# Kernel optimization log

Hardware: AMD Instinct MI355X
Metric: run time of the kernel (lower is better)

The kernel has to match this reference:

```python
import jax, jax.numpy as jnp
import numpy as np

B, Z, K, T = 4, 64, 400, 48000
CIN, COUT, KS, DIL = 128, 128, 3, 1
H = 32


def setup_inputs() -> dict:
    key = jax.random.key(0)
    ks = jax.random.split(key, 10)
    s = lambda n: 1.0 / np.sqrt(n)
    return {
        "x": jax.random.normal(ks[0], (B, CIN, T), jnp.float32),
        "z": jax.random.normal(ks[1], (B, Z, K), jnp.float32),
        # weight_model: Conv1d(Z->H, k=1), ReLU, Conv1d(H -> CIN*COUT*KS, k=1)
        "w1": jax.random.normal(ks[2], (H, Z), jnp.float32) * s(Z),
        "b1": jax.random.normal(ks[3], (H,), jnp.float32) * 0.01,
        "w2": jax.random.normal(ks[4], (CIN * COUT * KS, H), jnp.float32) * s(H),
        "b2": jax.random.normal(ks[5], (CIN * COUT * KS,), jnp.float32) * s(CIN * KS),
        # bias_model: Conv1d(Z->H, k=1), ReLU, Conv1d(H -> COUT, k=1)
        "bw1": jax.random.normal(ks[6], (H, Z), jnp.float32) * s(Z),
        "bb1": jax.random.normal(ks[7], (H,), jnp.float32) * 0.01,
        "bw2": jax.random.normal(ks[8], (COUT, H), jnp.float32) * s(H),
        "bb2": jax.random.normal(ks[9], (COUT,), jnp.float32) * 0.01,
    }


def _mlp1x1(z, wa, ba, wb, bb):
    # two pointwise Conv1d layers with ReLU in between; z: [B, Z, K]
    h = jax.nn.relu(jnp.einsum('hz,bzk->bhk', wa, z) + ba[None, :, None])
    return jnp.einsum('oh,bhk->bok', wb, h) + bb[None, :, None]


def _unfold_causal(x, ksize, dil):
    # causal im2col: tap i is x delayed by i*dil samples (left-padded with zeros)
    pad = dil * (ksize - 1)
    xp = jnp.pad(x, ((0, 0), (0, 0), (pad, 0)))
    taps = [xp[:, :, pad - i * dil: pad - i * dil + x.shape[-1]] for i in range(ksize)]
    return jnp.concatenate(taps, axis=1)  # [B, CIN*KS, T]


def reference(x, z, w1, b1, w2, b2, bw1, bb1, bw2, bb2):
    Tk = T // K  # samples per weight chunk
    xu = _unfold_causal(x, KS, DIL)                       # [B, CIN*KS, T]
    xr = xu.transpose(0, 2, 1).reshape(B * K, Tk, CIN * KS)
    w = _mlp1x1(z, w1, b1, w2, b2)                        # [B, CIN*COUT*KS, K]
    w = w.reshape(B, CIN * KS, COUT, K).transpose(0, 3, 1, 2).reshape(B * K, CIN * KS, COUT)
    bias = _mlp1x1(z, bw1, bb1, bw2, bb2)                 # [B, COUT, K]
    bias = bias.transpose(0, 2, 1).reshape(B * K, COUT)
    y = jnp.einsum('btc,bco->bto', xr, w) + bias[:, None, :]
    return y.reshape(B, T, COUT).transpose(0, 2, 1)       # [B, COUT, T]
```

## Files before the change

kernel.cpp:

```cpp
#include <hip/hip_runtime.h>
#include <stdint.h>

#define TT     48000
#define TK     120
#define NC     128
#define NA     384
#define NZ     64
#define NH     32
#define NK     400
#define NCHUNK 1600
#define MW     49152

typedef float f32x4 __attribute__((ext_vector_type(4)));
typedef __bf16 bf16x8 __attribute__((ext_vector_type(8)));

static __device__ __forceinline__ uint16_t f2bf(float f) {
    uint32_t x; __builtin_memcpy(&x, &f, 4);
    return (uint16_t)((x + 0x7fffu + ((x >> 16) & 1u)) >> 16);
}
static __device__ __forceinline__ uint32_t pk2u(uint16_t lo, uint16_t hi) {
    return (uint32_t)lo | ((uint32_t)hi << 16);
}

__global__ __launch_bounds__(256) void k1_hidden(
    const float* __restrict__ z,
    const float* __restrict__ w1, const float* __restrict__ b1,
    const float* __restrict__ bw1, const float* __restrict__ bb1,
    const float* __restrict__ bw2, const float* __restrict__ bb2,
    uint16_t* __restrict__ Hb, float* __restrict__ biasws) {
    int tid = threadIdx.x, lane = tid & 63, w = tid >> 6;
    int chunk0 = blockIdx.x * 4;
    int b = chunk0 / NK;
    int k0 = chunk0 - b * NK;

    __shared__ float w1sT[64][33];
    __shared__ float bw1sT[64][33];
    __shared__ float bw2s[128][33];
    __shared__ float zs[64][4];
    __shared__ float hbs[4][33];
    __shared__ float b1s[32], bb1s[32], bb2s[128];

    {
        int row = tid >> 3, c0 = (tid & 7) * 8;
        float4 a0 = *(const float4*)(w1 + row * NZ + c0);
        float4 a1 = *(const float4*)(w1 + row * NZ + c0 + 4);
        float4 c0v = *(const float4*)(bw1 + row * NZ + c0);
        float4 c1v = *(const float4*)(bw1 + row * NZ + c0 + 4);
        const float av[8] = {a0.x,a0.y,a0.z,a0.w,a1.x,a1.y,a1.z,a1.w};
        const float cv[8] = {c0v.x,c0v.y,c0v.z,c0v.w,c1v.x,c1v.y,c1v.z,c1v.w};
#pragma unroll
        for (int j = 0; j < 8; ++j) {
            w1sT[c0 + j][row]  = av[j];
            bw1sT[c0 + j][row] = cv[j];
        }
    }
    {
        int r = tid >> 1, cb = (tid & 1) * 16;
        float4 v0 = *(const float4*)(bw2 + r * NH + cb);
        float4 v1 = *(const float4*)(bw2 + r * NH + cb + 4);
        float4 v2 = *(const float4*)(bw2 + r * NH + cb + 8);
        float4 v3 = *(const float4*)(bw2 + r * NH + cb + 12);
        const float vv[16] = {v0.x,v0.y,v0.z,v0.w,v1.x,v1.y,v1.z,v1.w,
                              v2.x,v2.y,v2.z,v2.w,v3.x,v3.y,v3.z,v3.w};
#pragma unroll
        for (int j = 0; j < 16; ++j) bw2s[r][cb + j] = vv[j];
    }
    if (tid < 64) {
        float4 zv = *(const float4*)(z + ((size_t)b * NZ + tid) * NK + k0);
        zs[tid][0] = zv.x; zs[tid][1] = zv.y; zs[tid][2] = zv.z; zs[tid][3] = zv.w;
    }
    if (tid < 32) { b1s[tid] = b1[tid]; bb1s[tid] = bb1[tid]; }
    if (tid >= 128 && tid < 256) bb2s[tid - 128] = bb2[tid - 128];
    __syncthreads();

    int chunk = chunk0 + w;
    if (lane < NH) {
        float s = b1s[lane];
#pragma unroll
        for (int i = 0; i < NZ; ++i) s = fmaf(w1sT[i][lane], zs[i][w], s);
        Hb[(size_t)chunk * NH + lane] = f2bf(fmaxf(s, 0.f));
    } else {
        int j = lane - NH;
        float s = bb1s[j];
#pragma unroll
        for (int i = 0; i < NZ; ++i) s = fmaf(bw1sT[i][j], zs[i][w], s);
        hbs[w][j] = fmaxf(s, 0.f);
    }

#pragma unroll
    for (int r = 0; r < 2; ++r) {
        int c = r * 64 + lane;
        float s = bb2s[c];
#pragma unroll
        for (int j = 0; j < NH; ++j) s = fmaf(bw2s[c][j], hbs[w][j], s);
        biasws[(size_t)chunk * NC + c] = s;
    }
}

__global__ __launch_bounds__(256) void k2_wgen(
    const float* __restrict__ w2, const float* __restrict__ b2,
    const uint16_t* __restrict__ Hb, uint16_t* __restrict__ Wt,
    int chunk0, int nchunk) {
    int tid = threadIdx.x, lane = tid & 63, w = tid >> 6;
    int quad = lane >> 4, li = lane & 15;
    __shared__ __align__(16) uint16_t St[4][16][68];
    int mb = blockIdx.x * 256 + w * 64;

    bf16x8 afrag[4];
    float4 bias[4];
#pragma unroll
    for (int t = 0; t < 4; ++t) {
        int mp = mb + t * 16 + li;
        int a = mp % NA, c = mp / NA;
        const float* src = w2 + ((size_t)a * NC + c) * NH + quad * 8;
        float4 v0 = *(const float4*)(src);
        float4 v1 = *(const float4*)(src + 4);
        uint16_t tmp[8] = { f2bf(v0.x), f2bf(v0.y), f2bf(v0.z), f2bf(v0.w),
                            f2bf(v1.x), f2bf(v1.y), f2bf(v1.z), f2bf(v1.w) };
        __builtin_memcpy(&afrag[t], tmp, 16);
        float bv[4];
#pragma unroll
        for (int r = 0; r < 4; ++r) {
            int mpr = mb + t * 16 + quad * 4 + r;
            bv[r] = b2[(size_t)(mpr % NA) * NC + (mpr / NA)];
        }
        bias[t] = make_float4(bv[0], bv[1], bv[2], bv[3]);
    }

    for (int g = 0; g < 10; ++g) {
        int cl0 = blockIdx.y * 160 + g * 16;
        if (cl0 >= nchunk) break;
        int cl = cl0 + li;
        if (cl >= nchunk) cl = nchunk - 1;
        bf16x8 hfrag = *(const bf16x8*)(Hb + (size_t)(chunk0 + cl) * NH + quad * 8);
#pragma unroll
        for (int t = 0; t < 4; ++t) {
            f32x4 acc = {0.f, 0.f, 0.f, 0.f};
            acc = __builtin_amdgcn_mfma_f32_16x16x32_bf16(afrag[t], hfrag, acc, 0, 0, 0);
            uint16_t p[4] = { f2bf(acc[0] + bias[t].x), f2bf(acc[1] + bias[t].y),
                              f2bf(acc[2] + bias[t].z), f2bf(acc[3] + bias[t].w) };
            uint64_t pv; __builtin_memcpy(&pv, p, 8);
            *(uint64_t*)&St[w][li][t * 16 + quad * 4] = pv;
        }
#pragma unroll
        for (int p = 0; p < 2; ++p) {
            int ch = (lane >> 3) + p * 8, part = lane & 7;
            uint4 v = *(const uint4*)&St[w][ch][part * 8];
            int cg = cl0 + ch;
            if (cg < nchunk)
                *(uint4*)(Wt + (size_t)cg * MW + mb + part * 8) = v;
        }
    }
}

__global__ __launch_bounds__(512, 4) void k3_conv(
    const float* __restrict__ x, const uint16_t* __restrict__ Wt,
    const float* __restrict__ biasws, float* __restrict__ out, int chunk0) {
    int cl = blockIdx.x, chunk = chunk0 + cl;
    int b = chunk / NK, k = chunk - b * NK;
    int kbase = k * TK;
    int tid = threadIdx.x, lane = tid & 63, w = tid >> 6;
    int quad = lane >> 4, li = lane & 15;
    int tblk = (w >> 1) * 32, cblk = (w & 1) * 64;

    __shared__ __align__(16) char smem[81920];
    char* Xa  = smem;
    char* Db0 = smem + 32768;
    char* Db1 = smem + 49152;
    char* Db2 = smem + 65536;
    const uint16_t* WtC = Wt + (size_t)cl * MW;

    auto stageD = [&](char* dst, int dks) {
#pragma unroll
        for (int j = 0; j < 2; ++j) {
            int g = (w * 2 + j) * 64 + lane;
            int c = g >> 3, sd = g & 7;
            int o = sd ^ (c & 7);
            const uint16_t* gsrc = WtC + (size_t)c * NA + dks * 64 + o * 8;
            __builtin_amdgcn_global_load_lds(
                (__attribute__((address_space(1))) void*)gsrc,
                (__attribute__((address_space(3))) void*)(dst + (w * 2 + j) * 1024),
                16, 0, 0);
        }
    };

    stageD(Db0, 0);
    stageD(Db1, 1);

    const float* xb = x + (size_t)b * NC * TT;
    {
        int thalf = lane >> 5;
        int tq4 = (lane & 31) * 4;
#pragma unroll
        for (int i = 0; i < 4; ++i) {
            int p = i * 16 + w * 2 + thalf;
            int cin = p * 2;
            int tg = kbase + tq4;
            int tga = tg > TT - 4 ? TT - 4 : tg;
            float4 v0 = *(const float4*)(xb + (size_t)cin * TT + tga);
            float4 v1 = *(const float4*)(xb + (size_t)(cin + 1) * TT + tga);
            uint32_t pks[4] = { pk2u(f2bf(v0.x), f2bf(v1.x)),
                                pk2u(f2bf(v0.y), f2bf(v1.y)),
                                pk2u(f2bf(v0.z), f2bf(v1.z)),
                                pk2u(f2bf(v0.w), f2bf(v1.w)) };
            int q = cin >> 3, wi = (cin & 7) * 2;
#pragma unroll
            for (int j = 0; j < 4; ++j) {
                int r = tq4 + 2 + j;
                if (r < 128)
                    *(uint32_t*)(Xa + r * 256 + ((q ^ (r & 15)) << 4) + wi) = pks[j];
            }
            if (tq4 == 0) {
                uint32_t r0 = 0, r1 = 0;
                if (kbase > 0) {
                    float2 u0 = *(const float2*)(xb + (size_t)cin * TT + kbase - 2);
                    float2 u1 = *(const float2*)(xb + (size_t)(cin + 1) * TT + kbase - 2);
                    r0 = pk2u(f2bf(u0.x), f2bf(u1.x));
                    r1 = pk2u(f2bf(u0.y), f2bf(u1.y));
                }
                *(uint32_t*)(Xa + (q << 4) + wi) = r0;
                *(uint32_t*)(Xa + 256 + ((q ^ 1) << 4) + wi) = r1;
            }
        }
    }
    asm volatile("s_waitcnt lgkmcnt(0)" ::: "memory");

    f32x4 acc[2][4];
#pragma unroll
    for (int i = 0; i < 2; ++i)
#pragma unroll
        for (int j = 0; j < 4; ++j) acc[i][j] = (f32x4){0.f, 0.f, 0.f, 0.f};

#pragma unroll
    for (int dk = 0; dk < 6; ++dk) {
        if (dk < 5) asm volatile("s_waitcnt vmcnt(2)" ::: "memory");
        else        asm volatile("s_waitcnt vmcnt(0)" ::: "memory");
        __builtin_amdgcn_s_barrier();
        __builtin_amdgcn_sched_barrier(0);
        if (dk < 4) {
            int sel = (dk + 2) % 3;
            stageD(sel == 0 ? Db0 : (sel == 1 ? Db1 : Db2), dk + 2);
        }
        int cs = dk % 3;
        char* cur = cs == 0 ? Db0 : (cs == 1 ? Db1 : Db2);
        int tap = dk >> 1;

        bf16x8 bfr[2][4];
#pragma unroll
        for (int s = 0; s < 2; ++s)
#pragma unroll
            for (int ct = 0; ct < 4; ++ct) {
                int c = cblk + ct * 16 + li;
                bfr[s][ct] = *(const bf16x8*)(cur + c * 128
                             + (((s * 4 + quad) ^ (c & 7)) << 4));
            }
#pragma unroll
        for (int s = 0; s < 2; ++s) {
            bf16x8 af[2];
#pragma unroll
            for (int tt = 0; tt < 2; ++tt) {
                int r = tblk + tt * 16 + li + 2 - tap;
                r = r > 127 ? 127 : r;
                int q = (dk & 1) * 8 + s * 4 + quad;
                af[tt] = *(const bf16x8*)(Xa + r * 256 + ((q ^ (r & 15)) << 4));
            }
#pragma unroll
            for (int tt = 0; tt < 2; ++tt)
#pragma unroll
                for (int ct = 0; ct < 4; ++ct)
                    acc[tt][ct] = __builtin_amdgcn_mfma_f32_16x16x32_bf16(
                        af[tt], bfr[s][ct], acc[tt][ct], 0, 0, 0);
        }
    }

#pragma unroll
    for (int ct = 0; ct < 4; ++ct) {
        int c = cblk + ct * 16 + li;
        float bias = biasws[(size_t)chunk * NC + c];
        float* ob = out + ((size_t)b * NC + c) * TT + kbase;
#pragma unroll
        for (int tt = 0; tt < 2; ++tt) {
            int t0v = tblk + tt * 16 + quad * 4;
            if (t0v < TK) {
                f32x4 v = acc[tt][ct];
                *(float4*)(ob + t0v) = make_float4(v[0] + bias, v[1] + bias,
                                                   v[2] + bias, v[3] + bias);
            }
        }
    }
}

extern "C" void kernel_launch(void* const* d_in, const int* in_sizes, int n_in,
                              void* d_out, int out_size, void* d_ws, size_t ws_size,
                              hipStream_t stream) {
    const float* x   = (const float*)d_in[0];
    const float* z   = (const float*)d_in[1];
    const float* w1  = (const float*)d_in[2];
    const float* b1  = (const float*)d_in[3];
    const float* w2  = (const float*)d_in[4];
    const float* b2  = (const float*)d_in[5];
    const float* bw1 = (const float*)d_in[6];
    const float* bb1 = (const float*)d_in[7];
    const float* bw2 = (const float*)d_in[8];
    const float* bb2 = (const float*)d_in[9];
    float* out = (float*)d_out;

    char* ws = (char*)d_ws;
    uint16_t* Hb     = (uint16_t*)(ws);
    float*    biasws = (float*)(ws + 102400);
    const size_t wt_off = 921600;
    uint16_t* Wt     = (uint16_t*)(ws + wt_off);

    size_t avail = (ws_size > wt_off) ? (ws_size - wt_off) : 0;
    int batch = (int)(avail / ((size_t)MW * 2));
    if (batch > 800) batch = 800;
    if (batch < 1) batch = 1;

    k1_hidden<<<NCHUNK / 4, 256, 0, stream>>>(z, w1, b1, bw1, bb1, bw2, bb2, Hb, biasws);

    for (int c0 = 0; c0 < NCHUNK; c0 += batch) {
        int nc = NCHUNK - c0;
        if (nc > batch) nc = batch;
        dim3 g2(MW / 256, (nc + 159) / 160, 1);
        k2_wgen<<<g2, 256, 0, stream>>>(w2, b2, Hb, Wt, c0, nc);
        k3_conv<<<nc, 512, 0, stream>>>(x, Wt, biasws, out, c0);
    }
}
```

Measured before the change: 284.6 us.

## Load conv weights directly into registers, drop LDS weight staging

The conv kernel now reads its per-chunk weight fragments straight from global memory into registers, double-buffered in software across the six K-steps, instead of staging them through three LDS buffers with async global-to-LDS loads and per-step barriers. LDS use falls from 80 KB to 32 KB (only the input tile), and the launch bound is raised to allow 8 blocks per CU. This is meant to remove per-step barriers and LDS traffic and to raise occupancy. In exchange, each wave issues its own global loads for weights (64 channels are duplicated across the four t-block waves), and register pressure goes up.

```diff
diff --git a/kernel.cpp b/kernel.cpp
--- a/kernel.cpp
+++ b/kernel.cpp
@@ -153,7 +153,7 @@
     }
 }
 
-__global__ __launch_bounds__(512, 4) void k3_conv(
+__global__ __launch_bounds__(512, 8) void k3_conv(
     const float* __restrict__ x, const uint16_t* __restrict__ Wt,
     const float* __restrict__ biasws, float* __restrict__ out, int chunk0) {
     int cl = blockIdx.x, chunk = chunk0 + cl;
@@ -163,29 +163,21 @@
     int quad = lane >> 4, li = lane & 15;
     int tblk = (w >> 1) * 32, cblk = (w & 1) * 64;
 
-    __shared__ __align__(16) char smem[81920];
-    char* Xa  = smem;
-    char* Db0 = smem + 32768;
-    char* Db1 = smem + 49152;
-    char* Db2 = smem + 65536;
+    __shared__ __align__(16) char Xa[32768];
     const uint16_t* WtC = Wt + (size_t)cl * MW;
 
-    auto stageD = [&](char* dst, int dks) {
-#pragma unroll
-        for (int j = 0; j < 2; ++j) {
-            int g = (w * 2 + j) * 64 + lane;
-            int c = g >> 3, sd = g & 7;
-            int o = sd ^ (c & 7);
-            const uint16_t* gsrc = WtC + (size_t)c * NA + dks * 64 + o * 8;
-            __builtin_amdgcn_global_load_lds(
-                (__attribute__((address_space(1))) void*)gsrc,
-                (__attribute__((address_space(3))) void*)(dst + (w * 2 + j) * 1024),
-                16, 0, 0);
-        }
-    };
-
-    stageD(Db0, 0);
-    stageD(Db1, 1);
+    const uint16_t* wsrc = WtC + (size_t)(cblk + li) * NA + quad * 8;
+
+#define LOADW(dst, dk)                                                        \
+    _Pragma("unroll")                                                         \
+    for (int s = 0; s < 2; ++s)                                               \
+        _Pragma("unroll")                                                     \
+        for (int ct = 0; ct < 4; ++ct)                                        \
+            dst[s][ct] = *(const bf16x8*)(wsrc + (size_t)ct * 16 * NA         \
+                                          + (dk) * 64 + s * 32);
+
+    bf16x8 w0[2][4], w1[2][4];
+    LOADW(w0, 0);
 
     const float* xb = x + (size_t)b * NC * TT;
     {
@@ -223,7 +215,7 @@
             }
         }
     }
-    asm volatile("s_waitcnt lgkmcnt(0)" ::: "memory");
+    __syncthreads();
 
     f32x4 acc[2][4];
 #pragma unroll
@@ -231,47 +223,33 @@
 #pragma unroll
         for (int j = 0; j < 4; ++j) acc[i][j] = (f32x4){0.f, 0.f, 0.f, 0.f};
 
-#pragma unroll
-    for (int dk = 0; dk < 6; ++dk) {
-        if (dk < 5) asm volatile("s_waitcnt vmcnt(2)" ::: "memory");
-        else        asm volatile("s_waitcnt vmcnt(0)" ::: "memory");
-        __builtin_amdgcn_s_barrier();
-        __builtin_amdgcn_sched_barrier(0);
-        if (dk < 4) {
-            int sel = (dk + 2) % 3;
-            stageD(sel == 0 ? Db0 : (sel == 1 ? Db1 : Db2), dk + 2);
-        }
-        int cs = dk % 3;
-        char* cur = cs == 0 ? Db0 : (cs == 1 ? Db1 : Db2);
-        int tap = dk >> 1;
-
-        bf16x8 bfr[2][4];
-#pragma unroll
-        for (int s = 0; s < 2; ++s)
-#pragma unroll
-            for (int ct = 0; ct < 4; ++ct) {
-                int c = cblk + ct * 16 + li;
-                bfr[s][ct] = *(const bf16x8*)(cur + c * 128
-                             + (((s * 4 + quad) ^ (c & 7)) << 4));
-            }
-#pragma unroll
-        for (int s = 0; s < 2; ++s) {
-            bf16x8 af[2];
-#pragma unroll
-            for (int tt = 0; tt < 2; ++tt) {
-                int r = tblk + tt * 16 + li + 2 - tap;
-                r = r > 127 ? 127 : r;
-                int q = (dk & 1) * 8 + s * 4 + quad;
-                af[tt] = *(const bf16x8*)(Xa + r * 256 + ((q ^ (r & 15)) << 4));
-            }
-#pragma unroll
-            for (int tt = 0; tt < 2; ++tt)
-#pragma unroll
-                for (int ct = 0; ct < 4; ++ct)
-                    acc[tt][ct] = __builtin_amdgcn_mfma_f32_16x16x32_bf16(
-                        af[tt], bfr[s][ct], acc[tt][ct], 0, 0, 0);
-        }
-    }
+#define MSTEP(wf, dk)                                                         \
+    _Pragma("unroll")                                                         \
+    for (int s = 0; s < 2; ++s) {                                             \
+        bf16x8 af[2];                                                         \
+        _Pragma("unroll")                                                     \
+        for (int tt = 0; tt < 2; ++tt) {                                      \
+            int r = tblk + tt * 16 + li + 2 - ((dk) >> 1);                    \
+            r = r > 127 ? 127 : r;                                            \
+            int q = ((dk) & 1) * 8 + s * 4 + quad;                            \
+            af[tt] = *(const bf16x8*)(Xa + r * 256 + ((q ^ (r & 15)) << 4));  \
+        }                                                                     \
+        _Pragma("unroll")                                                     \
+        for (int tt = 0; tt < 2; ++tt)                                        \
+            _Pragma("unroll")                                                 \
+            for (int ct = 0; ct < 4; ++ct)                                    \
+                acc[tt][ct] = __builtin_amdgcn_mfma_f32_16x16x32_bf16(        \
+                    af[tt], wf[s][ct], acc[tt][ct], 0, 0, 0);                 \
+    }
+
+    LOADW(w1, 1);  MSTEP(w0, 0);
+    LOADW(w0, 2);  MSTEP(w1, 1);
+    LOADW(w1, 3);  MSTEP(w0, 2);
+    LOADW(w0, 4);  MSTEP(w1, 3);
+    LOADW(w1, 5);  MSTEP(w0, 4);
+                   MSTEP(w1, 5);
+#undef LOADW
+#undef MSTEP
 
 #pragma unroll
     for (int ct = 0; ct < 4; ++ct) {
```

New measurement: 463.9 us. 1.63x slower.
